# Performance work log

Measured on AMD Instinct MI355X. Metric: run time of the kernel, lower is better.

Reference implementation:

```python
import jax, jax.numpy as jnp
import numpy as np

NC, C, D = 64, 256, 32
K, K_b = 16, 16
ALPHA, B = 16, 16
H_S, H_M, H_MOD = 128, 128, 32
N = NC * C
BS = 8


def setup_inputs() -> dict:
    key = jax.random.key(0)
    ks = jax.random.split(key, 20)
    f32 = jnp.float32
    state_in, msg_in = 3 * D + 1, 3 * D
    mod_in, mod_out = K + 3 * D + 1, K + K_b + 1 + D
    inp = {}
    inp['x'] = jax.random.normal(ks[0], (BS, NC * D), f32)
    inp['h'] = jax.random.normal(ks[1], (BS, NC, C, D), f32) * 0.1
    inp['prev_messages'] = jax.random.normal(ks[2], (BS, NC, C, D), f32) * 0.1
    inp['decay_logit'] = jax.random.normal(ks[3], (BS, NC, C), f32) * 0.1
    inp['primitives_state'] = jax.random.normal(ks[4], (BS, NC, C, D), f32) * 0.1
    inp['hebbian_traces'] = jax.random.normal(ks[5], (BS, NC, C, K), f32) * 0.1
    inp['hebbian_traces_border'] = jax.random.normal(ks[6], (BS, NC, B, K_b), f32) * 0.1
    inp['state_w1'] = jax.random.normal(ks[7], (H_S, state_in), f32) * (2.0 / (state_in + H_S)) ** 0.5
    inp['state_b1'] = jnp.zeros((H_S,), f32)
    inp['state_w2'] = jax.random.normal(ks[8], (D, H_S), f32) * (2.0 / (H_S + D)) ** 0.5
    inp['state_b2'] = jnp.zeros((D,), f32)
    inp['msg_w1'] = jax.random.normal(ks[9], (H_M, msg_in), f32) * (2.0 / (msg_in + H_M)) ** 0.5
    inp['msg_b1'] = jnp.zeros((H_M,), f32)
    inp['msg_w2'] = jax.random.normal(ks[10], (D, H_M), f32) * (2.0 / (H_M + D)) ** 0.5
    inp['msg_b2'] = jnp.zeros((D,), f32)
    inp['mod_w1'] = jax.random.normal(ks[11], (N, H_MOD, mod_in), f32) * (2.0 / (mod_in + H_MOD)) ** 0.5
    inp['mod_b1'] = jnp.zeros((N, H_MOD), f32)
    inp['mod_w2'] = jax.random.normal(ks[12], (N, H_MOD, mod_out), f32) * (2.0 / (H_MOD + mod_out)) ** 0.5
    inp['mod_b2'] = jnp.zeros((N, mod_out), f32)
    inp['neuron_id'] = jax.random.normal(ks[13], (NC, C, D), f32) * D ** -0.5
    inp['conn_indices'] = jax.random.randint(ks[14], (NC, C, K), 0, C)
    inp['border_conn_indices'] = jax.random.randint(ks[15], (NC, B, K_b), 0, NC * B)
    return inp


def reference(x, h, prev_messages, decay_logit, primitives_state,
              hebbian_traces, hebbian_traces_border,
              state_w1, state_b1, state_w2, state_b2,
              msg_w1, msg_b1, msg_w2, msg_b2,
              mod_w1, mod_b1, mod_w2, mod_b2,
              neuron_id, conn_indices, border_conn_indices):
    bs = x.shape[0]
    # inject: [BS, NC*D] -> add to first ALPHA neurons of each cell
    inj = x.reshape(bs, NC, D)
    h = h.at[:, :, :ALPHA, :].add(inj[:, :, None, :])

    # per-neuron modulator (each of N=NC*C neurons has its own 2-layer MLP)
    nid = jnp.broadcast_to(neuron_id[None], (bs, NC, C, D))
    mod_input = jnp.concatenate(
        [hebbian_traces, h, decay_logit[..., None], primitives_state, nid], axis=-1)
    flat = mod_input.reshape(bs, N, -1)                       # [bs, N, mod_in]
    hid = jnp.tanh(jnp.einsum('bni,nhi->bnh', flat, mod_w1) + mod_b1)
    out = jnp.einsum('bnh,nho->bno', hid, mod_w2) + mod_b2    # [bs, N, mod_out]
    out = out.reshape(bs, NC, C, -1)
    new_w_conn = out[..., :K]                                 # [bs,NC,C,K]
    new_w_conn_border = out[..., K:K + K_b][:, :, ALPHA:ALPHA + B, :]
    new_decay = out[..., K + K_b]                             # [bs,NC,C]
    new_prim = out[..., K + K_b + 1:]                         # [bs,NC,C,D]

    # cell-local weighted gather over conn_indices
    cell_idx = jnp.arange(NC)[:, None, None]
    neigh = prev_messages[:, cell_idx, conn_indices]          # [bs,NC,C,K,D]
    w_sig = jax.nn.sigmoid(new_w_conn + hebbian_traces)
    agg = jnp.einsum('bnck,bnckd->bncd', w_sig, neigh)

    # inter-cell border gather over border_conn_indices
    border_flat = prev_messages[:, :, ALPHA:ALPHA + B, :].reshape(bs, NC * B, D)
    conn_flat = border_conn_indices.reshape(NC * B, K_b)
    bneigh = border_flat[:, conn_flat].reshape(bs, NC, B, K_b, D)
    wb_sig = jax.nn.sigmoid(new_w_conn_border + hebbian_traces_border)
    bagg = jnp.einsum('bnck,bnckd->bncd', wb_sig, bneigh)
    agg = agg.at[:, :, ALPHA:ALPHA + B, :].add(bagg)

    # shared state MLP (in = 3D+1) with learned decay gate
    sin = jnp.concatenate([h, agg, new_prim, new_decay[..., None]], axis=-1)
    shid = jnp.tanh(jnp.einsum('bnci,hi->bnch', sin, state_w1) + state_b1)
    delta = jnp.einsum('bnch,dh->bncd', shid, state_w2) + state_b2
    decay = jax.nn.sigmoid(new_decay)[..., None]
    h_new = decay * h + (1.0 - decay) * jnp.tanh(delta)

    # shared message MLP (in = 3D)
    min_ = jnp.concatenate([h_new, agg, nid], axis=-1)
    mhid = jnp.tanh(jnp.einsum('bnci,hi->bnch', min_, msg_w1) + msg_b1)
    msg = jnp.einsum('bnch,dh->bncd', mhid, msg_w2) + msg_b2

    # Hebbian trace updates (pre = gathered neighbor msgs, post = new msg)
    heb = 0.9 * hebbian_traces + 0.1 * jnp.einsum('bncd,bnckd->bnck', msg, neigh) / D
    msg_b = msg[:, :, ALPHA:ALPHA + B, :]
    heb_b = 0.9 * hebbian_traces_border + 0.1 * jnp.einsum('bncd,bnckd->bnck', msg_b, bneigh) / D

    # readout from last ALPHA neurons of each cell
    readout = msg[:, :, C - ALPHA:, :].mean(axis=2).reshape(bs, NC * D)
    return readout, h_new, msg, heb, heb_b
```

## Files before the change

kernel.cpp:

```cpp
#include <hip/hip_runtime.h>

#define NCC   64
#define CCH   256
#define DD    32
#define KK    16
#define KBB   16
#define AL    16
#define BRD   16
#define NTOT  16384
#define BSZ   8
#define WSROW 68

#ifndef __has_builtin
#define __has_builtin(x) 0
#endif
#if __has_builtin(__builtin_amdgcn_fdot2)
#define HAVE_FDOT2 1
#else
#define HAVE_FDOT2 0
#endif

typedef unsigned int uint32;
typedef __fp16 half2v __attribute__((ext_vector_type(2)));
union HU { half2v h; uint32 u; };

struct __align__(4) F4u { float a0, a1, a2, a3; };
struct __align__(4) F2u { float a, b; };
__device__ __forceinline__ F4u ld4u(const float* __restrict__ p) {
    return *reinterpret_cast<const F4u*>(p);
}
__device__ __forceinline__ float fsig(float v) { return 1.0f / (1.0f + __expf(-v)); }
__device__ __forceinline__ float ftanhf(float v) {
    return 1.0f - 2.0f / (__expf(2.0f * v) + 1.0f);
}
__device__ __forceinline__ uint32 packpair(float a, float b) {
    HU cv; cv.h = __builtin_amdgcn_cvt_pkrtz(a, b);
    return cv.u;
}
__device__ __forceinline__ void unpackpair(uint32 u, float& a, float& b) {
    HU cv; cv.u = u;
    a = (float)cv.h.x; b = (float)cv.h.y;
}
__device__ __forceinline__ float dot2(uint32 x, uint32 w, float c) {
    HU a, b; a.u = x; b.u = w;
#if HAVE_FDOT2
    return __builtin_amdgcn_fdot2(a.h, b.h, c, false);
#else
    return c + (float)a.h.x * (float)b.h.x + (float)a.h.y * (float)b.h.y;
#endif
}

__global__ __launch_bounds__(256) void kA(
    const float* __restrict__ x, const float* __restrict__ h_in,
    const float* __restrict__ dlog, const float* __restrict__ prim,
    const float* __restrict__ heb, const float* __restrict__ nidp,
    const float* __restrict__ mw1, const float* __restrict__ mb1,
    const float* __restrict__ mw2, const float* __restrict__ mb2,
    float* __restrict__ outw)
{
    __shared__ __align__(16) float s_flat[8][8][116];
    __shared__ __align__(16) float s_hid[8][32][8];

    const int tid = threadIdx.x;
    const int n0  = blockIdx.x * 8;
    const int nc  = n0 >> 8;
    const int c0  = n0 & 255;

    for (int e = tid; e < 8 * 8 * 116; e += 256) {
        const int nl = e / (8 * 116);
        const int rr = e - nl * (8 * 116);
        const int b  = rr / 116;
        const int i  = rr - b * 116;
        const int c  = c0 + nl;
        const int row = (b * NCC + nc) * CCH + c;
        float v;
        if (i < 16)        v = heb[(size_t)row * KK + i];
        else if (i < 48) { const int d = i - 16;
                           v = h_in[(size_t)row * DD + d]
                             + (c < AL ? x[(size_t)(b * NCC + nc) * DD + d] : 0.0f); }
        else if (i == 48)  v = dlog[row];
        else if (i < 81)   v = prim[(size_t)row * DD + (i - 49)];
        else if (i < 113)  v = nidp[(size_t)(nc * CCH + c) * DD + (i - 81)];
        else               v = 0.0f;
        s_flat[nl][b][i] = v;
    }
    __syncthreads();

    const int nl = tid >> 5;
    const int n  = n0 + nl;

    {
        const int h = tid & 31;
        const float* __restrict__ w1row = mw1 + ((size_t)n * 32 + h) * 113;
        const float bias = mb1[n * 32 + h];
        float acc[8];
        #pragma unroll
        for (int b = 0; b < 8; ++b) acc[b] = bias;
        #pragma unroll
        for (int i = 0; i < 112; i += 4) {
            F4u w = ld4u(w1row + i);
            #pragma unroll
            for (int b = 0; b < 8; ++b) {
                float4 xv = *(const float4*)&s_flat[nl][b][i];
                acc[b] += w.a0*xv.x + w.a1*xv.y + w.a2*xv.z + w.a3*xv.w;
            }
        }
        const float wt = w1row[112];
        #pragma unroll
        for (int b = 0; b < 8; ++b) acc[b] += wt * s_flat[nl][b][112];
        float4 t0 = make_float4(ftanhf(acc[0]), ftanhf(acc[1]), ftanhf(acc[2]), ftanhf(acc[3]));
        float4 t1 = make_float4(ftanhf(acc[4]), ftanhf(acc[5]), ftanhf(acc[6]), ftanhf(acc[7]));
        *(float4*)&s_hid[nl][h][0] = t0;
        *(float4*)&s_hid[nl][h][4] = t1;
    }
    __syncthreads();

    {
        const int o2 = tid & 31;
        const float* __restrict__ w2base = mw2 + (size_t)n * (32 * 65);
        float acc0[8], acc1[8];
        {
            const float bz0 = mb2[n * 65 + 2 * o2];
            const float bz1 = mb2[n * 65 + 2 * o2 + 1];
            #pragma unroll
            for (int b = 0; b < 8; ++b) { acc0[b] = bz0; acc1[b] = bz1; }
        }
        #pragma unroll 4
        for (int hh = 0; hh < 32; ++hh) {
            F2u w = *(const F2u*)(w2base + hh * 65 + 2 * o2);
            float4 hA = *(const float4*)&s_hid[nl][hh][0];
            float4 hB = *(const float4*)&s_hid[nl][hh][4];
            acc0[0] += w.a*hA.x; acc0[1] += w.a*hA.y; acc0[2] += w.a*hA.z; acc0[3] += w.a*hA.w;
            acc0[4] += w.a*hB.x; acc0[5] += w.a*hB.y; acc0[6] += w.a*hB.z; acc0[7] += w.a*hB.w;
            acc1[0] += w.b*hA.x; acc1[1] += w.b*hA.y; acc1[2] += w.b*hA.z; acc1[3] += w.b*hA.w;
            acc1[4] += w.b*hB.x; acc1[5] += w.b*hB.y; acc1[6] += w.b*hB.z; acc1[7] += w.b*hB.w;
        }
        #pragma unroll
        for (int b = 0; b < 8; ++b) {
            float* row = outw + ((size_t)b * NTOT + n) * WSROW;
            *(float2*)(row + 2 * o2) = make_float2(acc0[b], acc1[b]);
        }
        if (o2 == 31) {
            float a64[8];
            const float bz = mb2[n * 65 + 64];
            #pragma unroll
            for (int b = 0; b < 8; ++b) a64[b] = bz;
            for (int hh = 0; hh < 32; ++hh) {
                const float wv = w2base[hh * 65 + 64];
                float4 hA = *(const float4*)&s_hid[nl][hh][0];
                float4 hB = *(const float4*)&s_hid[nl][hh][4];
                a64[0] += wv*hA.x; a64[1] += wv*hA.y; a64[2] += wv*hA.z; a64[3] += wv*hA.w;
                a64[4] += wv*hB.x; a64[5] += wv*hB.y; a64[6] += wv*hB.z; a64[7] += wv*hB.w;
            }
            #pragma unroll
            for (int b = 0; b < 8; ++b)
                outw[((size_t)b * NTOT + n) * WSROW + 64] = a64[b];
        }
    }
}

__device__ __forceinline__ void stageW(int tid, const float* __restrict__ w1g, int n1,
                                       const float* __restrict__ b1g,
                                       const float* __restrict__ w2g,
                                       const float* __restrict__ b2g,
                                       uint32 (*w1buf)[52], uint32 (*w2buf)[64],
                                       float* b1buf, float* b2buf)
{
    for (int t = tid; t < 128 * 52; t += 256) {
        const int hh = t / 52;
        const int p  = t - hh * 52;
        const int e0 = 2 * p, e1 = 2 * p + 1;
        const float f0 = (e0 < n1) ? w1g[hh * n1 + e0] : 0.0f;
        const float f1 = (e1 < n1) ? w1g[hh * n1 + e1] : 0.0f;
        w1buf[hh][p] = packpair(f0, f1);
    }
    for (int t = tid; t < 32 * 64; t += 256) {
        const int d = t >> 6;
        const int p = t & 63;
        w2buf[d][p] = packpair(w2g[d * 128 + 2 * p], w2g[d * 128 + 2 * p + 1]);
    }
    if (tid < 128) b1buf[tid] = b1g[tid];
    if (tid < 32)  b2buf[tid] = b2g[tid];
}

__device__ __forceinline__ void mlp2(const uint32* xin,
                                     const uint32 (*w1)[52], const uint32 (*w2)[64],
                                     const float* b1, const float* b2, float* out)
{
    #pragma unroll
    for (int d = 0; d < 32; ++d) out[d] = b2[d];
    #pragma unroll 1
    for (int hc = 0; hc < 16; ++hc) {
        float sh[8];
        #pragma unroll
        for (int jj = 0; jj < 8; ++jj) {
            const int h = hc * 8 + jj;
            float a = b1[h];
            #pragma unroll
            for (int p = 0; p < 13; ++p) {
                uint4 wq = *(const uint4*)&w1[h][p * 4];
                a = dot2(xin[p*4+0], wq.x, a);
                a = dot2(xin[p*4+1], wq.y, a);
                a = dot2(xin[p*4+2], wq.z, a);
                a = dot2(xin[p*4+3], wq.w, a);
            }
            sh[jj] = ftanhf(a);
        }
        uint32 shp[4];
        #pragma unroll
        for (int q = 0; q < 4; ++q) shp[q] = packpair(sh[2*q], sh[2*q+1]);
        #pragma unroll
        for (int d = 0; d < 32; ++d) {
            uint4 wq = *(const uint4*)&w2[d][hc * 4];
            float a = out[d];
            a = dot2(shp[0], wq.x, a);
            a = dot2(shp[1], wq.y, a);
            a = dot2(shp[2], wq.z, a);
            a = dot2(shp[3], wq.w, a);
            out[d] = a;
        }
    }
}

__global__ __launch_bounds__(256) void kB(
    const float* __restrict__ x, const float* __restrict__ h_in,
    const float* __restrict__ prev, const float* __restrict__ heb_in,
    const float* __restrict__ hebb_in,
    const float* __restrict__ sw1, const float* __restrict__ sb1,
    const float* __restrict__ sw2, const float* __restrict__ sb2,
    const float* __restrict__ qw1, const float* __restrict__ qb1,
    const float* __restrict__ qw2, const float* __restrict__ qb2,
    const float* __restrict__ nidp,
    const int* __restrict__ conn, const int* __restrict__ bconn,
    const float* __restrict__ wsm,
    float* __restrict__ o_hnew, float* __restrict__ o_msg,
    float* __restrict__ o_heb, float* __restrict__ o_hebb)
{
    __shared__ __align__(16) uint32 w1buf[128][52];
    __shared__ __align__(16) uint32 w2buf[32][64];
    __shared__ float b1buf[128];
    __shared__ float b2buf[32];

    const int tid = threadIdx.x;
    const int r  = blockIdx.x * 256 + tid;
    const int b  = r >> 14;
    const int n  = r & (NTOT - 1);
    const int nc = n >> 8;
    const int c  = n & 255;
    const int cellbase = (b * NCC + nc) * CCH;

    stageW(tid, sw1, 97, sb1, sw2, sb2, w1buf, w2buf, b1buf, b2buf);
    __syncthreads();

    float ovw[16], ovb[16], decayl;
    uint32 xs[52];
    {
        const float4* op4 = (const float4*)(wsm + (size_t)r * WSROW);
        #pragma unroll
        for (int q = 0; q < 4; ++q) {
            float4 t = op4[q];
            ovw[q*4+0]=t.x; ovw[q*4+1]=t.y; ovw[q*4+2]=t.z; ovw[q*4+3]=t.w;
        }
        #pragma unroll
        for (int q = 0; q < 4; ++q) {
            float4 t = op4[4 + q];
            ovb[q*4+0]=t.x; ovb[q*4+1]=t.y; ovb[q*4+2]=t.z; ovb[q*4+3]=t.w;
        }
        float tail[36];
        #pragma unroll
        for (int q = 0; q < 9; ++q) {
            float4 t = op4[8 + q];
            tail[q*4+0]=t.x; tail[q*4+1]=t.y; tail[q*4+2]=t.z; tail[q*4+3]=t.w;
        }
        decayl = tail[0];
        #pragma unroll
        for (int q = 0; q < 16; ++q)
            xs[32 + q] = packpair(tail[1 + 2*q], tail[2 + 2*q]);
        xs[48] = packpair(decayl, 0.0f);
        xs[49] = xs[50] = xs[51] = 0u;
    }
    {
        float hvf[32];
        const float4* hp = (const float4*)(h_in + (size_t)r * DD);
        #pragma unroll
        for (int q = 0; q < 8; ++q) {
            float4 t = hp[q];
            hvf[q*4+0]=t.x; hvf[q*4+1]=t.y; hvf[q*4+2]=t.z; hvf[q*4+3]=t.w;
        }
        if (c < AL) {
            const float4* xp = (const float4*)(x + (size_t)(b * NCC + nc) * DD);
            #pragma unroll
            for (int q = 0; q < 8; ++q) {
                float4 t = xp[q];
                hvf[q*4+0]+=t.x; hvf[q*4+1]+=t.y; hvf[q*4+2]+=t.z; hvf[q*4+3]+=t.w;
            }
        }
        #pragma unroll
        for (int q = 0; q < 16; ++q) xs[q] = packpair(hvf[2*q], hvf[2*q+1]);
    }
    float hb[16];
    {
        const float4* ep = (const float4*)(heb_in + (size_t)r * KK);
        #pragma unroll
        for (int q = 0; q < 4; ++q) {
            float4 t = ep[q];
            hb[q*4+0]=t.x; hb[q*4+1]=t.y; hb[q*4+2]=t.z; hb[q*4+3]=t.w;
        }
    }
    const bool isb = (c >= AL) && (c < AL + BRD);
    {
        float agg[32];
        #pragma unroll
        for (int d = 0; d < 32; ++d) agg[d] = 0.0f;
        const int4* cp = (const int4*)(conn + n * KK);
        #pragma unroll
        for (int q = 0; q < 4; ++q) {
            int4 ci = cp[q];
            int cis[4] = {ci.x, ci.y, ci.z, ci.w};
            #pragma unroll
            for (int kk = 0; kk < 4; ++kk) {
                const int k = q * 4 + kk;
                const float wk = fsig(ovw[k] + hb[k]);
                const float4* np = (const float4*)(prev + (size_t)(cellbase + cis[kk]) * DD);
                #pragma unroll
                for (int dq = 0; dq < 8; ++dq) {
                    float4 t = np[dq];
                    agg[dq*4+0] += wk*t.x; agg[dq*4+1] += wk*t.y;
                    agg[dq*4+2] += wk*t.z; agg[dq*4+3] += wk*t.w;
                }
            }
        }
        if (isb) {
            const int cb = c - AL;
            const int4*   bp  = (const int4*)(bconn + (nc * BRD + cb) * KBB);
            const float4* hp4 = (const float4*)(hebb_in + (size_t)((b * NCC + nc) * BRD + cb) * KBB);
            #pragma unroll
            for (int q = 0; q < 4; ++q) {
                int4 bi = bp[q];
                float4 hbt = hp4[q];
                int bis[4]   = {bi.x, bi.y, bi.z, bi.w};
                float hbs[4] = {hbt.x, hbt.y, hbt.z, hbt.w};
                #pragma unroll
                for (int kk = 0; kk < 4; ++kk) {
                    const int k   = q * 4 + kk;
                    const int idx = bis[kk];
                    const int nb  = idx >> 4;
                    const int ch  = AL + (idx & 15);
                    const float wk = fsig(ovb[k] + hbs[kk]);
                    const float4* np = (const float4*)(prev + (size_t)((b * NCC + nb) * CCH + ch) * DD);
                    #pragma unroll
                    for (int dq = 0; dq < 8; ++dq) {
                        float4 t = np[dq];
                        agg[dq*4+0] += wk*t.x; agg[dq*4+1] += wk*t.y;
                        agg[dq*4+2] += wk*t.z; agg[dq*4+3] += wk*t.w;
                    }
                }
            }
        }
        #pragma unroll
        for (int q = 0; q < 16; ++q) xs[16 + q] = packpair(agg[2*q], agg[2*q+1]);
    }

    uint32 hnp[16];
    {
        float delta[32];
        mlp2(xs, w1buf, w2buf, b1buf, b2buf, delta);
        const float sd = fsig(decayl);
        float* hrow = o_hnew + (size_t)r * DD;
        #pragma unroll
        for (int q = 0; q < 16; ++q) {
            float h0, h1;
            unpackpair(xs[q], h0, h1);
            const float t0 = sd * h0 + (1.0f - sd) * ftanhf(delta[2*q]);
            const float t1 = sd * h1 + (1.0f - sd) * ftanhf(delta[2*q+1]);
            hnp[q] = packpair(t0, t1);
            *(float2*)(hrow + 2*q) = make_float2(t0, t1);
        }
    }

    __syncthreads();
    stageW(tid, qw1, 96, qb1, qw2, qb2, w1buf, w2buf, b1buf, b2buf);
    __syncthreads();

    float macc[32];
    {
        uint32 xm[52];
        #pragma unroll
        for (int q = 0; q < 16; ++q) xm[q] = hnp[q];
        #pragma unroll
        for (int q = 0; q < 16; ++q) xm[16 + q] = xs[16 + q];
        const float4* npd = (const float4*)(nidp + (size_t)n * DD);
        #pragma unroll
        for (int q = 0; q < 8; ++q) {
            float4 t = npd[q];
            xm[32 + 2*q]     = packpair(t.x, t.y);
            xm[32 + 2*q + 1] = packpair(t.z, t.w);
        }
        xm[48] = xm[49] = xm[50] = xm[51] = 0u;
        mlp2(xm, w1buf, w2buf, b1buf, b2buf, macc);
        float4* mop = (float4*)(o_msg + (size_t)r * DD);
        #pragma unroll
        for (int q = 0; q < 8; ++q)
            mop[q] = make_float4(macc[q*4+0], macc[q*4+1], macc[q*4+2], macc[q*4+3]);
    }

    {
        const int4* cp = (const int4*)(conn + n * KK);
        #pragma unroll
        for (int q = 0; q < 4; ++q) {
            int4 ci = cp[q];
            int cis[4] = {ci.x, ci.y, ci.z, ci.w};
            float hres[4];
            #pragma unroll
            for (int kk = 0; kk < 4; ++kk) {
                const float4* np = (const float4*)(prev + (size_t)(cellbase + cis[kk]) * DD);
                float dot = 0.0f;
                #pragma unroll
                for (int dq = 0; dq < 8; ++dq) {
                    float4 t = np[dq];
                    dot += macc[dq*4+0]*t.x + macc[dq*4+1]*t.y
                         + macc[dq*4+2]*t.z + macc[dq*4+3]*t.w;
                }
                hres[kk] = 0.9f * hb[q*4+kk] + 0.003125f * dot;
            }
            *(float4*)(o_heb + (size_t)r * KK + q*4)
                = make_float4(hres[0], hres[1], hres[2], hres[3]);
        }
    }
    if (isb) {
        const int cb = c - AL;
        const int4*   bp  = (const int4*)(bconn + (nc * BRD + cb) * KBB);
        const float4* hp4 = (const float4*)(hebb_in + (size_t)((b * NCC + nc) * BRD + cb) * KBB);
        #pragma unroll
        for (int q = 0; q < 4; ++q) {
            int4 bi = bp[q];
            float4 hbt = hp4[q];
            int bis[4]   = {bi.x, bi.y, bi.z, bi.w};
            float hbs[4] = {hbt.x, hbt.y, hbt.z, hbt.w};
            float hres[4];
            #pragma unroll
            for (int kk = 0; kk < 4; ++kk) {
                const int idx = bis[kk];
                const int nb  = idx >> 4;
                const int ch  = AL + (idx & 15);
                const float4* np = (const float4*)(prev + (size_t)((b * NCC + nb) * CCH + ch) * DD);
                float dot = 0.0f;
                #pragma unroll
                for (int dq = 0; dq < 8; ++dq) {
                    float4 t = np[dq];
                    dot += macc[dq*4+0]*t.x + macc[dq*4+1]*t.y
                         + macc[dq*4+2]*t.z + macc[dq*4+3]*t.w;
                }
                hres[kk] = 0.9f * hbs[kk] + 0.003125f * dot;
            }
            *(float4*)(o_hebb + (size_t)((b * NCC + nc) * BRD + cb) * KBB + q*4)
                = make_float4(hres[0], hres[1], hres[2], hres[3]);
        }
    }
}

__global__ __launch_bounds__(256) void kC(const float* __restrict__ msg,
                                          float* __restrict__ ro)
{
    const int t = blockIdx.x * 256 + threadIdx.x;
    const int b   = t >> 11;
    const int rem = t & 2047;
    const int nc  = rem >> 5;
    const int d   = rem & 31;
    const float* mp = msg + (size_t)((b * NCC + nc) * CCH + (CCH - AL)) * DD + d;
    float s = 0.0f;
    #pragma unroll
    for (int j = 0; j < 16; ++j) s += mp[j * DD];
    ro[t] = s * (1.0f / 16.0f);
}

extern "C" void kernel_launch(void* const* d_in, const int* in_sizes, int n_in,
                              void* d_out, int out_size, void* d_ws, size_t ws_size,
                              hipStream_t stream) {
    const float* x     = (const float*)d_in[0];
    const float* h     = (const float*)d_in[1];
    const float* prev  = (const float*)d_in[2];
    const float* dlog  = (const float*)d_in[3];
    const float* prim  = (const float*)d_in[4];
    const float* heb   = (const float*)d_in[5];
    const float* hebb  = (const float*)d_in[6];
    const float* sw1   = (const float*)d_in[7];
    const float* sb1   = (const float*)d_in[8];
    const float* sw2   = (const float*)d_in[9];
    const float* sb2   = (const float*)d_in[10];
    const float* qw1   = (const float*)d_in[11];
    const float* qb1   = (const float*)d_in[12];
    const float* qw2   = (const float*)d_in[13];
    const float* qb2   = (const float*)d_in[14];
    const float* mw1   = (const float*)d_in[15];
    const float* mb1   = (const float*)d_in[16];
    const float* mw2   = (const float*)d_in[17];
    const float* mb2   = (const float*)d_in[18];
    const float* nid   = (const float*)d_in[19];
    const int*   conn  = (const int*)d_in[20];
    const int*   bconn = (const int*)d_in[21];

    float* out   = (float*)d_out;
    float* ro    = out;
    float* hnew  = out + 16384;
    float* msg   = hnew + 4194304;
    float* hebo  = msg + 4194304;
    float* hebbo = hebo + 2097152;
    float* ws    = (float*)d_ws;

    kA<<<NTOT / 8, 256, 0, stream>>>(x, h, dlog, prim, heb, nid, mw1, mb1, mw2, mb2, ws);
    kB<<<(BSZ * NTOT) / 256, 256, 0, stream>>>(x, h, prev, heb, hebb,
                                               sw1, sb1, sw2, sb2,
                                               qw1, qb1, qw2, qb2,
                                               nid, conn, bconn, ws,
                                               hnew, msg, hebo, hebbo);
    kC<<<64, 256, 0, stream>>>(msg, ro);
}
```

Measured before the change: 1.028 ms.

## Prepack shared MLP weights once; restructure per-neuron modulator kernel with staged weights

A new prologue kernel packs the shared state and message MLP weights into fp16 pairs in global device arrays, once per call. kB then reads them directly through the cache instead of restaging them into LDS twice per block with barriers, which also frees kB's shared memory for higher occupancy. Separately, kA now handles 2 neurons per block instead of 8, stages mw1 coalesced into LDS, and splits batches across threads to raise parallelism. Reading weights from global memory instead of LDS inside the hot MLP loop may raise latency, and kA now launches four times as many blocks.

```diff
diff --git a/kernel.cpp b/kernel.cpp
--- a/kernel.cpp
+++ b/kernel.cpp
@@ -50,6 +50,47 @@
 #endif
 }
 
+__device__ __align__(16) uint32 g_w1s[128][52];
+__device__ __align__(16) uint32 g_w2s[32][64];
+__device__ __align__(16) float  g_b1s[128];
+__device__ __align__(16) float  g_b2s[32];
+__device__ __align__(16) uint32 g_w1m[128][52];
+__device__ __align__(16) uint32 g_w2m[32][64];
+__device__ __align__(16) float  g_b1m[128];
+__device__ __align__(16) float  g_b2m[32];
+
+__global__ __launch_bounds__(256) void kP(
+    const float* __restrict__ sw1, const float* __restrict__ sb1,
+    const float* __restrict__ sw2, const float* __restrict__ sb2,
+    const float* __restrict__ qw1, const float* __restrict__ qb1,
+    const float* __restrict__ qw2, const float* __restrict__ qb2)
+{
+    const int tid = blockIdx.x * 256 + threadIdx.x;
+    for (int t = tid; t < 128 * 52; t += 2048) {
+        const int hh = t / 52;
+        const int p  = t - hh * 52;
+        const int e0 = 2 * p, e1 = 2 * p + 1;
+        {
+            const float f0 = (e0 < 97) ? sw1[hh * 97 + e0] : 0.0f;
+            const float f1 = (e1 < 97) ? sw1[hh * 97 + e1] : 0.0f;
+            g_w1s[hh][p] = packpair(f0, f1);
+        }
+        {
+            const float f0 = (e0 < 96) ? qw1[hh * 96 + e0] : 0.0f;
+            const float f1 = (e1 < 96) ? qw1[hh * 96 + e1] : 0.0f;
+            g_w1m[hh][p] = packpair(f0, f1);
+        }
+    }
+    for (int t = tid; t < 32 * 64; t += 2048) {
+        const int d = t >> 6;
+        const int p = t & 63;
+        g_w2s[d][p] = packpair(sw2[d * 128 + 2 * p], sw2[d * 128 + 2 * p + 1]);
+        g_w2m[d][p] = packpair(qw2[d * 128 + 2 * p], qw2[d * 128 + 2 * p + 1]);
+    }
+    if (tid < 128) { g_b1s[tid] = sb1[tid]; g_b1m[tid] = qb1[tid]; }
+    if (tid < 32)  { g_b2s[tid] = sb2[tid]; g_b2m[tid] = qb2[tid]; }
+}
+
 __global__ __launch_bounds__(256) void kA(
     const float* __restrict__ x, const float* __restrict__ h_in,
     const float* __restrict__ dlog, const float* __restrict__ prim,
@@ -58,15 +99,16 @@
     const float* __restrict__ mw2, const float* __restrict__ mb2,
     float* __restrict__ outw)
 {
-    __shared__ __align__(16) float s_flat[8][8][116];
-    __shared__ __align__(16) float s_hid[8][32][8];
+    __shared__ __align__(16) float s_flat[2][8][116];
+    __shared__ __align__(16) float s_w1[64][116];
+    __shared__ __align__(16) float s_hid[2][32][8];
 
     const int tid = threadIdx.x;
-    const int n0  = blockIdx.x * 8;
+    const int n0  = blockIdx.x * 2;
     const int nc  = n0 >> 8;
     const int c0  = n0 & 255;
 
-    for (int e = tid; e < 8 * 8 * 116; e += 256) {
+    for (int e = tid; e < 2 * 8 * 116; e += 256) {
         const int nl = e / (8 * 116);
         const int rr = e - nl * (8 * 116);
         const int b  = rr / 116;
@@ -84,108 +126,82 @@
         else               v = 0.0f;
         s_flat[nl][b][i] = v;
     }
+    {
+        const float* __restrict__ gw = mw1 + (size_t)n0 * (32 * 113);
+        for (int t = tid; t < 64 * 29; t += 256) {
+            const int r = t / 29;
+            const int c = t - r * 29;
+            if (c < 28) {
+                F4u v = ld4u(gw + r * 113 + c * 4);
+                *(float4*)&s_w1[r][c * 4] = make_float4(v.a0, v.a1, v.a2, v.a3);
+            } else {
+                const float v = gw[r * 113 + 112];
+                *(float4*)&s_w1[r][112] = make_float4(v, 0.0f, 0.0f, 0.0f);
+            }
+        }
+    }
     __syncthreads();
 
-    const int nl = tid >> 5;
+    const int nl = tid >> 7;
+    const int j  = (tid >> 2) & 31;
+    const int bq = tid & 3;
     const int n  = n0 + nl;
 
     {
-        const int h = tid & 31;
-        const float* __restrict__ w1row = mw1 + ((size_t)n * 32 + h) * 113;
-        const float bias = mb1[n * 32 + h];
-        float acc[8];
-        #pragma unroll
-        for (int b = 0; b < 8; ++b) acc[b] = bias;
-        #pragma unroll
-        for (int i = 0; i < 112; i += 4) {
-            F4u w = ld4u(w1row + i);
-            #pragma unroll
-            for (int b = 0; b < 8; ++b) {
-                float4 xv = *(const float4*)&s_flat[nl][b][i];
-                acc[b] += w.a0*xv.x + w.a1*xv.y + w.a2*xv.z + w.a3*xv.w;
-            }
-        }
-        const float wt = w1row[112];
-        #pragma unroll
-        for (int b = 0; b < 8; ++b) acc[b] += wt * s_flat[nl][b][112];
-        float4 t0 = make_float4(ftanhf(acc[0]), ftanhf(acc[1]), ftanhf(acc[2]), ftanhf(acc[3]));
-        float4 t1 = make_float4(ftanhf(acc[4]), ftanhf(acc[5]), ftanhf(acc[6]), ftanhf(acc[7]));
-        *(float4*)&s_hid[nl][h][0] = t0;
-        *(float4*)&s_hid[nl][h][4] = t1;
+        const float bias = mb1[n * 32 + j];
+        float acc0 = bias, acc1 = bias;
+        const float* __restrict__ wr = &s_w1[nl * 32 + j][0];
+        #pragma unroll
+        for (int c = 0; c < 29; ++c) {
+            float4 w  = *(const float4*)(wr + c * 4);
+            float4 x0 = *(const float4*)&s_flat[nl][2 * bq][c * 4];
+            float4 x1 = *(const float4*)&s_flat[nl][2 * bq + 1][c * 4];
+            acc0 += w.x * x0.x + w.y * x0.y + w.z * x0.z + w.w * x0.w;
+            acc1 += w.x * x1.x + w.y * x1.y + w.z * x1.z + w.w * x1.w;
+        }
+        *(float2*)&s_hid[nl][j][2 * bq] = make_float2(ftanhf(acc0), ftanhf(acc1));
     }
     __syncthreads();
 
     {
-        const int o2 = tid & 31;
         const float* __restrict__ w2base = mw2 + (size_t)n * (32 * 65);
-        float acc0[8], acc1[8];
-        {
-            const float bz0 = mb2[n * 65 + 2 * o2];
-            const float bz1 = mb2[n * 65 + 2 * o2 + 1];
-            #pragma unroll
-            for (int b = 0; b < 8; ++b) { acc0[b] = bz0; acc1[b] = bz1; }
-        }
+        const float bz0 = mb2[n * 65 + 2 * j];
+        const float bz1 = mb2[n * 65 + 2 * j + 1];
+        float a0[2] = {bz0, bz0};
+        float a1[2] = {bz1, bz1};
         #pragma unroll 4
         for (int hh = 0; hh < 32; ++hh) {
-            F2u w = *(const F2u*)(w2base + hh * 65 + 2 * o2);
-            float4 hA = *(const float4*)&s_hid[nl][hh][0];
-            float4 hB = *(const float4*)&s_hid[nl][hh][4];
-            acc0[0] += w.a*hA.x; acc0[1] += w.a*hA.y; acc0[2] += w.a*hA.z; acc0[3] += w.a*hA.w;
-            acc0[4] += w.a*hB.x; acc0[5] += w.a*hB.y; acc0[6] += w.a*hB.z; acc0[7] += w.a*hB.w;
-            acc1[0] += w.b*hA.x; acc1[1] += w.b*hA.y; acc1[2] += w.b*hA.z; acc1[3] += w.b*hA.w;
-            acc1[4] += w.b*hB.x; acc1[5] += w.b*hB.y; acc1[6] += w.b*hB.z; acc1[7] += w.b*hB.w;
-        }
-        #pragma unroll
-        for (int b = 0; b < 8; ++b) {
+            F2u w = *(const F2u*)(w2base + hh * 65 + 2 * j);
+            float2 hv = *(const float2*)&s_hid[nl][hh][2 * bq];
+            a0[0] += w.a * hv.x; a0[1] += w.a * hv.y;
+            a1[0] += w.b * hv.x; a1[1] += w.b * hv.y;
+        }
+        #pragma unroll
+        for (int bb = 0; bb < 2; ++bb) {
+            const int b = 2 * bq + bb;
             float* row = outw + ((size_t)b * NTOT + n) * WSROW;
-            *(float2*)(row + 2 * o2) = make_float2(acc0[b], acc1[b]);
-        }
-        if (o2 == 31) {
-            float a64[8];
+            *(float2*)(row + 2 * j) = make_float2(a0[bb], a1[bb]);
+        }
+        if (j == 31) {
             const float bz = mb2[n * 65 + 64];
-            #pragma unroll
-            for (int b = 0; b < 8; ++b) a64[b] = bz;
+            float a64[2] = {bz, bz};
             for (int hh = 0; hh < 32; ++hh) {
                 const float wv = w2base[hh * 65 + 64];
-                float4 hA = *(const float4*)&s_hid[nl][hh][0];
-                float4 hB = *(const float4*)&s_hid[nl][hh][4];
-                a64[0] += wv*hA.x; a64[1] += wv*hA.y; a64[2] += wv*hA.z; a64[3] += wv*hA.w;
-                a64[4] += wv*hB.x; a64[5] += wv*hB.y; a64[6] += wv*hB.z; a64[7] += wv*hB.w;
-            }
-            #pragma unroll
-            for (int b = 0; b < 8; ++b)
-                outw[((size_t)b * NTOT + n) * WSROW + 64] = a64[b];
-        }
-    }
-}
-
-__device__ __forceinline__ void stageW(int tid, const float* __restrict__ w1g, int n1,
-                                       const float* __restrict__ b1g,
-                                       const float* __restrict__ w2g,
-                                       const float* __restrict__ b2g,
-                                       uint32 (*w1buf)[52], uint32 (*w2buf)[64],
-                                       float* b1buf, float* b2buf)
-{
-    for (int t = tid; t < 128 * 52; t += 256) {
-        const int hh = t / 52;
-        const int p  = t - hh * 52;
-        const int e0 = 2 * p, e1 = 2 * p + 1;
-        const float f0 = (e0 < n1) ? w1g[hh * n1 + e0] : 0.0f;
-        const float f1 = (e1 < n1) ? w1g[hh * n1 + e1] : 0.0f;
-        w1buf[hh][p] = packpair(f0, f1);
-    }
-    for (int t = tid; t < 32 * 64; t += 256) {
-        const int d = t >> 6;
-        const int p = t & 63;
-        w2buf[d][p] = packpair(w2g[d * 128 + 2 * p], w2g[d * 128 + 2 * p + 1]);
-    }
-    if (tid < 128) b1buf[tid] = b1g[tid];
-    if (tid < 32)  b2buf[tid] = b2g[tid];
-}
-
-__device__ __forceinline__ void mlp2(const uint32* xin,
-                                     const uint32 (*w1)[52], const uint32 (*w2)[64],
-                                     const float* b1, const float* b2, float* out)
+                float2 hv = *(const float2*)&s_hid[nl][hh][2 * bq];
+                a64[0] += wv * hv.x; a64[1] += wv * hv.y;
+            }
+            #pragma unroll
+            for (int bb = 0; bb < 2; ++bb)
+                outw[((size_t)(2 * bq + bb) * NTOT + n) * WSROW + 64] = a64[bb];
+        }
+    }
+}
+
+__device__ __forceinline__ void mlp2g(const uint32* xin,
+                                      const uint32 (* __restrict__ w1)[52],
+                                      const uint32 (* __restrict__ w2)[64],
+                                      const float* __restrict__ b1,
+                                      const float* __restrict__ b2, float* out)
 {
     #pragma unroll
     for (int d = 0; d < 32; ++d) out[d] = b2[d];
@@ -226,21 +242,12 @@
     const float* __restrict__ x, const float* __restrict__ h_in,
     const float* __restrict__ prev, const float* __restrict__ heb_in,
     const float* __restrict__ hebb_in,
-    const float* __restrict__ sw1, const float* __restrict__ sb1,
-    const float* __restrict__ sw2, const float* __restrict__ sb2,
-    const float* __restrict__ qw1, const float* __restrict__ qb1,
-    const float* __restrict__ qw2, const float* __restrict__ qb2,
     const float* __restrict__ nidp,
     const int* __restrict__ conn, const int* __restrict__ bconn,
     const float* __restrict__ wsm,
     float* __restrict__ o_hnew, float* __restrict__ o_msg,
     float* __restrict__ o_heb, float* __restrict__ o_hebb)
 {
-    __shared__ __align__(16) uint32 w1buf[128][52];
-    __shared__ __align__(16) uint32 w2buf[32][64];
-    __shared__ float b1buf[128];
-    __shared__ float b2buf[32];
-
     const int tid = threadIdx.x;
     const int r  = blockIdx.x * 256 + tid;
     const int b  = r >> 14;
@@ -248,9 +255,6 @@
     const int nc = n >> 8;
     const int c  = n & 255;
     const int cellbase = (b * NCC + nc) * CCH;
-
-    stageW(tid, sw1, 97, sb1, sw2, sb2, w1buf, w2buf, b1buf, b2buf);
-    __syncthreads();
 
     float ovw[16], ovb[16], decayl;
     uint32 xs[52];
@@ -364,7 +368,7 @@
     uint32 hnp[16];
     {
         float delta[32];
-        mlp2(xs, w1buf, w2buf, b1buf, b2buf, delta);
+        mlp2g(xs, g_w1s, g_w2s, g_b1s, g_b2s, delta);
         const float sd = fsig(decayl);
         float* hrow = o_hnew + (size_t)r * DD;
         #pragma unroll
@@ -378,10 +382,6 @@
         }
     }
 
-    __syncthreads();
-    stageW(tid, qw1, 96, qb1, qw2, qb2, w1buf, w2buf, b1buf, b2buf);
-    __syncthreads();
-
     float macc[32];
     {
         uint32 xm[52];
@@ -397,7 +397,7 @@
             xm[32 + 2*q + 1] = packpair(t.z, t.w);
         }
         xm[48] = xm[49] = xm[50] = xm[51] = 0u;
-        mlp2(xm, w1buf, w2buf, b1buf, b2buf, macc);
+        mlp2g(xm, g_w1m, g_w2m, g_b1m, g_b2m, macc);
         float4* mop = (float4*)(o_msg + (size_t)r * DD);
         #pragma unroll
         for (int q = 0; q < 8; ++q)
@@ -508,10 +508,9 @@
     float* hebbo = hebo + 2097152;
     float* ws    = (float*)d_ws;
 
-    kA<<<NTOT / 8, 256, 0, stream>>>(x, h, dlog, prim, heb, nid, mw1, mb1, mw2, mb2, ws);
+    kP<<<8, 256, 0, stream>>>(sw1, sb1, sw2, sb2, qw1, qb1, qw2, qb2);
+    kA<<<NTOT / 2, 256, 0, stream>>>(x, h, dlog, prim, heb, nid, mw1, mb1, mw2, mb2, ws);
     kB<<<(BSZ * NTOT) / 256, 256, 0, stream>>>(x, h, prev, heb, hebb,
-                                               sw1, sb1, sw2, sb2,
-                                               qw1, qb1, qw2, qb2,
                                                nid, conn, bconn, ws,
                                                hnew, msg, hebo, hebbo);
     kC<<<64, 256, 0, stream>>>(msg, ro);
```

After: 1.153 ms. 12.2% more time.

## Split per-neuron modulator MLP into two kernels with one neuron per block

Applied to the files above, without the earlier changes.

Replaces the single modulator kernel (8 neurons per block, per-thread 8-batch register tiles) with two kernels. The first computes hidden activations with one thread per (hidden, batch) pair and writes them to a scratch area borrowed from the msg output buffer. The second stages the second-layer weights into shared memory with float4 loads and computes the outputs one thread per (output, batch). The goal is more parallelism and coalesced weight loads, paid for with an extra launch, a global round trip for hidden activations, and more blocks.

```diff
diff --git a/kernel.cpp b/kernel.cpp
--- a/kernel.cpp
+++ b/kernel.cpp
@@ -50,28 +50,23 @@
 #endif
 }
 
-__global__ __launch_bounds__(256) void kA(
+__global__ __launch_bounds__(256) void kA1(
     const float* __restrict__ x, const float* __restrict__ h_in,
     const float* __restrict__ dlog, const float* __restrict__ prim,
     const float* __restrict__ heb, const float* __restrict__ nidp,
     const float* __restrict__ mw1, const float* __restrict__ mb1,
-    const float* __restrict__ mw2, const float* __restrict__ mb2,
-    float* __restrict__ outw)
-{
-    __shared__ __align__(16) float s_flat[8][8][116];
-    __shared__ __align__(16) float s_hid[8][32][8];
+    float* __restrict__ hidout)
+{
+    __shared__ __align__(16) float s_flat[8][116];
 
     const int tid = threadIdx.x;
-    const int n0  = blockIdx.x * 8;
-    const int nc  = n0 >> 8;
-    const int c0  = n0 & 255;
-
-    for (int e = tid; e < 8 * 8 * 116; e += 256) {
-        const int nl = e / (8 * 116);
-        const int rr = e - nl * (8 * 116);
-        const int b  = rr / 116;
-        const int i  = rr - b * 116;
-        const int c  = c0 + nl;
+    const int n   = blockIdx.x;
+    const int nc  = n >> 8;
+    const int c   = n & 255;
+
+    for (int e = tid; e < 8 * 116; e += 256) {
+        const int b = e / 116;
+        const int i = e - b * 116;
         const int row = (b * NCC + nc) * CCH + c;
         float v;
         if (i < 16)        v = heb[(size_t)row * KK + i];
@@ -82,80 +77,52 @@
         else if (i < 81)   v = prim[(size_t)row * DD + (i - 49)];
         else if (i < 113)  v = nidp[(size_t)(nc * CCH + c) * DD + (i - 81)];
         else               v = 0.0f;
-        s_flat[nl][b][i] = v;
+        s_flat[b][i] = v;
     }
     __syncthreads();
 
-    const int nl = tid >> 5;
-    const int n  = n0 + nl;
-
-    {
-        const int h = tid & 31;
-        const float* __restrict__ w1row = mw1 + ((size_t)n * 32 + h) * 113;
-        const float bias = mb1[n * 32 + h];
-        float acc[8];
-        #pragma unroll
-        for (int b = 0; b < 8; ++b) acc[b] = bias;
-        #pragma unroll
-        for (int i = 0; i < 112; i += 4) {
-            F4u w = ld4u(w1row + i);
-            #pragma unroll
-            for (int b = 0; b < 8; ++b) {
-                float4 xv = *(const float4*)&s_flat[nl][b][i];
-                acc[b] += w.a0*xv.x + w.a1*xv.y + w.a2*xv.z + w.a3*xv.w;
-            }
-        }
-        const float wt = w1row[112];
-        #pragma unroll
-        for (int b = 0; b < 8; ++b) acc[b] += wt * s_flat[nl][b][112];
-        float4 t0 = make_float4(ftanhf(acc[0]), ftanhf(acc[1]), ftanhf(acc[2]), ftanhf(acc[3]));
-        float4 t1 = make_float4(ftanhf(acc[4]), ftanhf(acc[5]), ftanhf(acc[6]), ftanhf(acc[7]));
-        *(float4*)&s_hid[nl][h][0] = t0;
-        *(float4*)&s_hid[nl][h][4] = t1;
+    const int h = tid >> 3;
+    const int b = tid & 7;
+    const float* __restrict__ wr = mw1 + ((size_t)n * 32 + h) * 113;
+    float acc = mb1[n * 32 + h];
+    #pragma unroll
+    for (int cq = 0; cq < 28; ++cq) {
+        F4u w = ld4u(wr + cq * 4);
+        float4 xv = *(const float4*)&s_flat[b][cq * 4];
+        acc += w.a0 * xv.x + w.a1 * xv.y + w.a2 * xv.z + w.a3 * xv.w;
+    }
+    acc += wr[112] * s_flat[b][112];
+    hidout[(size_t)n * 256 + tid] = ftanhf(acc);
+}
+
+__global__ __launch_bounds__(256) void kA2(
+    const float* __restrict__ hidin,
+    const float* __restrict__ mw2, const float* __restrict__ mb2,
+    float* __restrict__ outw)
+{
+    __shared__ __align__(16) float s_w2[32 * 65];
+    __shared__ __align__(16) float s_h2[256];
+
+    const int tid = threadIdx.x;
+    const int n   = blockIdx.x;
+
+    {
+        const float4* src = (const float4*)(mw2 + (size_t)n * (32 * 65));
+        float4* dst = (float4*)s_w2;
+        for (int u = tid; u < 520; u += 256) dst[u] = src[u];
+        if (tid < 64)
+            ((float4*)s_h2)[tid] = ((const float4*)(hidin + (size_t)n * 256))[tid];
     }
     __syncthreads();
 
-    {
-        const int o2 = tid & 31;
-        const float* __restrict__ w2base = mw2 + (size_t)n * (32 * 65);
-        float acc0[8], acc1[8];
-        {
-            const float bz0 = mb2[n * 65 + 2 * o2];
-            const float bz1 = mb2[n * 65 + 2 * o2 + 1];
-            #pragma unroll
-            for (int b = 0; b < 8; ++b) { acc0[b] = bz0; acc1[b] = bz1; }
-        }
-        #pragma unroll 4
-        for (int hh = 0; hh < 32; ++hh) {
-            F2u w = *(const F2u*)(w2base + hh * 65 + 2 * o2);
-            float4 hA = *(const float4*)&s_hid[nl][hh][0];
-            float4 hB = *(const float4*)&s_hid[nl][hh][4];
-            acc0[0] += w.a*hA.x; acc0[1] += w.a*hA.y; acc0[2] += w.a*hA.z; acc0[3] += w.a*hA.w;
-            acc0[4] += w.a*hB.x; acc0[5] += w.a*hB.y; acc0[6] += w.a*hB.z; acc0[7] += w.a*hB.w;
-            acc1[0] += w.b*hA.x; acc1[1] += w.b*hA.y; acc1[2] += w.b*hA.z; acc1[3] += w.b*hA.w;
-            acc1[4] += w.b*hB.x; acc1[5] += w.b*hB.y; acc1[6] += w.b*hB.z; acc1[7] += w.b*hB.w;
-        }
-        #pragma unroll
-        for (int b = 0; b < 8; ++b) {
-            float* row = outw + ((size_t)b * NTOT + n) * WSROW;
-            *(float2*)(row + 2 * o2) = make_float2(acc0[b], acc1[b]);
-        }
-        if (o2 == 31) {
-            float a64[8];
-            const float bz = mb2[n * 65 + 64];
-            #pragma unroll
-            for (int b = 0; b < 8; ++b) a64[b] = bz;
-            for (int hh = 0; hh < 32; ++hh) {
-                const float wv = w2base[hh * 65 + 64];
-                float4 hA = *(const float4*)&s_hid[nl][hh][0];
-                float4 hB = *(const float4*)&s_hid[nl][hh][4];
-                a64[0] += wv*hA.x; a64[1] += wv*hA.y; a64[2] += wv*hA.z; a64[3] += wv*hA.w;
-                a64[4] += wv*hB.x; a64[5] += wv*hB.y; a64[6] += wv*hB.z; a64[7] += wv*hB.w;
-            }
-            #pragma unroll
-            for (int b = 0; b < 8; ++b)
-                outw[((size_t)b * NTOT + n) * WSROW + 64] = a64[b];
-        }
+    for (int it = tid; it < 520; it += 256) {
+        const int o = it >> 3;
+        const int b = it & 7;
+        float acc = mb2[n * 65 + o];
+        #pragma unroll 8
+        for (int hh = 0; hh < 32; ++hh)
+            acc += s_w2[hh * 65 + o] * s_h2[hh * 8 + b];
+        outw[((size_t)b * NTOT + n) * WSROW + o] = acc;
     }
 }
 
@@ -508,7 +475,10 @@
     float* hebbo = hebo + 2097152;
     float* ws    = (float*)d_ws;
 
-    kA<<<NTOT / 8, 256, 0, stream>>>(x, h, dlog, prim, heb, nid, mw1, mb1, mw2, mb2, ws);
+    float* hidscratch = msg;
+
+    kA1<<<NTOT, 256, 0, stream>>>(x, h, dlog, prim, heb, nid, mw1, mb1, hidscratch);
+    kA2<<<NTOT, 256, 0, stream>>>(hidscratch, mw2, mb2, ws);
     kB<<<(BSZ * NTOT) / 256, 256, 0, stream>>>(x, h, prev, heb, hebb,
                                                sw1, sb1, sw2, sb2,
                                                qw1, qb1, qw2, qb2,
```

After: 993.6 us. 3.3% less time.
